# Performance work log

Hardware: AMD Instinct MI355X
Metric: run time of the kernel (lower is better)

## Reference

```python
import jax, jax.numpy as jnp
import numpy as np

BS, H, S, D = 2, 16, 4096, 64
BLOCK = 64
STRIDE_C = 3
NEG = -10000.0


def _global_index(seq_len, block_size, stride_c):
    # static Longformer-style global pattern: first token of each block plus
    # the last `stride_c` tokens of each block
    r = np.arange(seq_len)
    rem = r % block_size
    return np.nonzero((rem == 0) | (rem >= block_size - stride_c))[0]


def setup_inputs() -> dict:
    key = jax.random.key(0)
    k1, k2, k3 = jax.random.split(key, 3)
    q = jax.random.normal(k1, (BS, H, S, D), dtype=jnp.float32)
    k = jax.random.normal(k2, (BS, H, S, D), dtype=jnp.float32)
    v = jax.random.normal(k3, (BS, H, S, D), dtype=jnp.float32)
    mask = jnp.ones((BS, S), dtype=jnp.float32)  # all tokens valid -> pattern is static
    return {"query": q, "key": k, "value": v, "mask": mask}


def reference(query, key, value, mask):
    bs, h, S, d = query.shape
    block = BLOCK
    nb = S // block  # seq_len chosen as multiple of block_size, so pad_len == 0
    g_idx = jnp.asarray(_global_index(S, block, STRIDE_C))  # [G]

    # ---- block-local attention scores ----
    bq = query.reshape(bs, h, nb, block, d)
    bk = key.reshape(bs, h, nb, block, d)
    local = jnp.einsum('bhnxd,bhnyd->bhnxy', bq, bk)  # [bs,h,nb,block,block]
    # additive key-side mask (per key position within each block)
    key_mask = jnp.where(mask == 0.0, NEG, 0.0).reshape(bs, 1, nb, 1, block)
    local = (local + key_mask).reshape(bs, h, S, block)

    # ---- global-token attention scores ----
    gk = key[:, :, g_idx, :]    # [bs,h,G,d]
    gv = value[:, :, g_idx, :]  # [bs,h,G,d]
    gscores = jnp.einsum('bhsd,bhgd->bhsg', query, gk)  # [bs,h,S,G]
    gmask = jnp.where(mask[:, g_idx] == 0.0, NEG, 0.0)[:, None, None, :]
    gscores = gscores + gmask

    # ---- joint softmax over [local block | global tokens] ----
    scores = jnp.concatenate([local, gscores], axis=-1)  # [bs,h,S,block+G]
    probs = jax.nn.softmax(scores.astype(jnp.float32), axis=-1)

    # ---- weighted sums ----
    lp = probs[..., :block].reshape(bs, h, nb, block, block)
    bv = value.reshape(bs, h, nb, block, d)
    lout = jnp.matmul(lp, bv).reshape(bs, h, S, d)
    gout = jnp.einsum('bhsg,bhgd->bhsd', probs[..., block:], gv)
    return lout + gout
```

## Files before the change

kernel.cpp:

```cpp
#include <hip/hip_runtime.h>

#define NEGV -10000.0f

typedef _Float16 f16x8 __attribute__((ext_vector_type(8)));
typedef _Float16 f16x2 __attribute__((ext_vector_type(2)));
typedef float floatx4 __attribute__((ext_vector_type(4)));

__device__ __forceinline__ int src_row(int key, int nblk) {
    if (key < 64) return nblk * 64 + key;
    int g = key - 64;
    int p = g & 3;
    return (g >> 2) * 64 + (p ? (60 + p) : 0);
}

__global__ __launch_bounds__(256, 4)
void sparse_attn_kernel(const float* __restrict__ Q, const float* __restrict__ K,
                        const float* __restrict__ V, const float* __restrict__ M,
                        float* __restrict__ O)
{
    const int x    = blockIdx.x;
    const int bh   = (x & 7) * 4 + ((x >> 3) >> 6);
    const int nblk = (x >> 3) & 63;
    const int b    = bh >> 4;

    const size_t hoff = (size_t)bh * (4096 * 64);
    const float* Qh = Q + hoff;
    const float* Kh = K + hoff;
    const float* Vh = V + hoff;
    float*       Oh = O + hoff;
    const float* Mb = M + (size_t)b * 4096;

    __shared__ _Float16 smem[20480];
    _Float16* Pbase  = smem;
    _Float16* VTbase = smem + 10240;

    const int tid  = threadIdx.x;
    const int lane = tid & 63;
    const int wv   = tid >> 6;
    const int m    = lane & 15;
    const int quad = lane >> 4;
    const int sgl  = lane ^ (lane >> 2);
    const int cg   = lane & 15;
    const int ppb  = ((wv << 2) + (lane >> 4) + ((cg >> 2) << 2)) & 15;

    float mv[5];
    #pragma unroll
    for (int s = 0; s < 5; ++s)
        mv[s] = (Mb[src_row(s * 64 + lane, nblk)] == 0.0f) ? NEGV : 0.0f;

    const int qrow = nblk * 64 + wv * 16 + m;
    f16x8 qf[2];
    #pragma unroll
    for (int c = 0; c < 2; ++c) {
        const float* src = Qh + (size_t)qrow * 64 + c * 32 + quad * 8;
        float4 f0 = *(const float4*)src;
        float4 f1 = *(const float4*)(src + 4);
        qf[c][0] = (_Float16)f0.x; qf[c][1] = (_Float16)f0.y;
        qf[c][2] = (_Float16)f0.z; qf[c][3] = (_Float16)f0.w;
        qf[c][4] = (_Float16)f1.x; qf[c][5] = (_Float16)f1.y;
        qf[c][6] = (_Float16)f1.z; qf[c][7] = (_Float16)f1.w;
    }

    #pragma unroll
    for (int it = 0; it < 10; ++it) {
        int S    = it * 256 + tid;
        int row  = ((S >> 7) * 16) + (S & 15);
        int col0 = ((S >> 6) & 1) * 32 + ((S & 63) >> 4) * 8;
        const float* src = Kh + (size_t)src_row(row, nblk) * 64 + col0;
        float4 f0 = *(const float4*)src;
        float4 f1 = *(const float4*)(src + 4);
        f16x8 o;
        o[0] = (_Float16)f0.x; o[1] = (_Float16)f0.y;
        o[2] = (_Float16)f0.z; o[3] = (_Float16)f0.w;
        o[4] = (_Float16)f1.x; o[5] = (_Float16)f1.y;
        o[6] = (_Float16)f1.z; o[7] = (_Float16)f1.w;
        *(f16x8*)(&smem[S * 8]) = o;
    }

    __syncthreads();

    floatx4 acc[20];
    #pragma unroll
    for (int t = 0; t < 20; ++t) {
        float ma = __shfl(mv[t >> 2], (t & 3) * 16 + m, 64);
        acc[t][0] = ma; acc[t][1] = ma; acc[t][2] = ma; acc[t][3] = ma;
    }
    #pragma unroll
    for (int t = 0; t < 20; ++t) {
        #pragma unroll
        for (int c = 0; c < 2; ++c) {
            f16x8 kf = *(const f16x8*)(&smem[(t * 2 + c) * 512 + lane * 8]);
            acc[t] = __builtin_amdgcn_mfma_f32_16x16x32_f16(qf[c], kf, acc[t], 0, 0, 0);
        }
    }

    float rmax[4] = {-3e38f, -3e38f, -3e38f, -3e38f};
    #pragma unroll
    for (int t = 0; t < 20; ++t)
        #pragma unroll
        for (int r = 0; r < 4; ++r)
            rmax[r] = fmaxf(rmax[r], acc[t][r]);
    #pragma unroll
    for (int off = 8; off >= 1; off >>= 1)
        #pragma unroll
        for (int r = 0; r < 4; ++r)
            rmax[r] = fmaxf(rmax[r], __shfl_xor(rmax[r], off, 64));
    float rsum[4] = {0.f, 0.f, 0.f, 0.f};
    #pragma unroll
    for (int t = 0; t < 20; ++t)
        #pragma unroll
        for (int r = 0; r < 4; ++r) {
            float e = __expf(acc[t][r] - rmax[r]);
            acc[t][r] = e;
            rsum[r] += e;
        }
    #pragma unroll
    for (int off = 8; off >= 1; off >>= 1)
        #pragma unroll
        for (int r = 0; r < 4; ++r)
            rsum[r] += __shfl_xor(rsum[r], off, 64);
    float rinv[4];
    #pragma unroll
    for (int r = 0; r < 4; ++r) rinv[r] = 1.0f / rsum[r];

    __syncthreads();

    #pragma unroll
    for (int tp = 0; tp < 10; ++tp) {
        int slab = wv * 5 + (tp >> 1);
        int gb   = ((tp & 1) * 2 + (m >> 3)) * 16 + quad * 4;
        #pragma unroll
        for (int r = 0; r < 4; ++r) {
            int g  = gb + r;
            int sg = g ^ (g >> 2);
            Pbase[slab * 512 + sg * 8 + (m & 7)] = (_Float16)acc[tp][r];
        }
    }
    #pragma unroll
    for (int s = 0; s < 5; ++s) {
        int rl = 2 * (s * 16 + ppb);
        float4 f0 = *(const float4*)(Vh + (size_t)src_row(rl,     nblk) * 64 + cg * 4);
        float4 f1 = *(const float4*)(Vh + (size_t)src_row(rl + 1, nblk) * 64 + cg * 4);
        int slab = (cg >> 2) * 5 + (rl >> 5);
        int gq   = ((rl & 31) >> 3) * 16;
        int j0   = rl & 7;
        f16x2 pk[4];
        pk[0][0] = (_Float16)f0.x; pk[0][1] = (_Float16)f1.x;
        pk[1][0] = (_Float16)f0.y; pk[1][1] = (_Float16)f1.y;
        pk[2][0] = (_Float16)f0.z; pk[2][1] = (_Float16)f1.z;
        pk[3][0] = (_Float16)f0.w; pk[3][1] = (_Float16)f1.w;
        #pragma unroll
        for (int e = 0; e < 4; ++e) {
            int g  = gq + (cg & 3) * 4 + e;
            int sg = g ^ (g >> 2);
            *(f16x2*)(&VTbase[slab * 512 + sg * 8 + j0]) = pk[e];
        }
    }

    __syncthreads();

    floatx4 oacc[4] = {};
    #pragma unroll
    for (int kc = 0; kc < 5; ++kc) {
        f16x8 pf = *(const f16x8*)(&Pbase[(wv * 5 + kc) * 512 + sgl * 8]);
        #pragma unroll
        for (int t = 0; t < 4; ++t) {
            f16x8 vf = *(const f16x8*)(&VTbase[(t * 5 + kc) * 512 + sgl * 8]);
            oacc[t] = __builtin_amdgcn_mfma_f32_16x16x32_f16(pf, vf, oacc[t], 0, 0, 0);
        }
    }

    __syncthreads();

    #pragma unroll
    for (int tp = 0; tp < 10; ++tp) {
        int slab = wv * 5 + (tp >> 1);
        int gb   = ((tp & 1) * 2 + (m >> 3)) * 16 + quad * 4;
        #pragma unroll
        for (int r = 0; r < 4; ++r) {
            int g  = gb + r;
            int sg = g ^ (g >> 2);
            Pbase[slab * 512 + sg * 8 + (m & 7)] = (_Float16)acc[10 + tp][r];
        }
    }
    #pragma unroll
    for (int s = 0; s < 5; ++s) {
        int rl  = 2 * (s * 16 + ppb);
        int key = 160 + rl;
        float4 f0 = *(const float4*)(Vh + (size_t)src_row(key,     nblk) * 64 + cg * 4);
        float4 f1 = *(const float4*)(Vh + (size_t)src_row(key + 1, nblk) * 64 + cg * 4);
        int slab = (cg >> 2) * 5 + (rl >> 5);
        int gq   = ((rl & 31) >> 3) * 16;
        int j0   = rl & 7;
        f16x2 pk[4];
        pk[0][0] = (_Float16)f0.x; pk[0][1] = (_Float16)f1.x;
        pk[1][0] = (_Float16)f0.y; pk[1][1] = (_Float16)f1.y;
        pk[2][0] = (_Float16)f0.z; pk[2][1] = (_Float16)f1.z;
        pk[3][0] = (_Float16)f0.w; pk[3][1] = (_Float16)f1.w;
        #pragma unroll
        for (int e = 0; e < 4; ++e) {
            int g  = gq + (cg & 3) * 4 + e;
            int sg = g ^ (g >> 2);
            *(f16x2*)(&VTbase[slab * 512 + sg * 8 + j0]) = pk[e];
        }
    }

    __syncthreads();

    #pragma unroll
    for (int kc = 0; kc < 5; ++kc) {
        f16x8 pf = *(const f16x8*)(&Pbase[(wv * 5 + kc) * 512 + sgl * 8]);
        #pragma unroll
        for (int t = 0; t < 4; ++t) {
            f16x8 vf = *(const f16x8*)(&VTbase[(t * 5 + kc) * 512 + sgl * 8]);
            oacc[t] = __builtin_amdgcn_mfma_f32_16x16x32_f16(pf, vf, oacc[t], 0, 0, 0);
        }
    }

    #pragma unroll
    for (int t = 0; t < 4; ++t)
        #pragma unroll
        for (int r = 0; r < 4; ++r)
            Oh[(size_t)(nblk * 64 + wv * 16 + quad * 4 + r) * 64 + t * 16 + m] =
                oacc[t][r] * rinv[r];
}

extern "C" void kernel_launch(void* const* d_in, const int* in_sizes, int n_in,
                              void* d_out, int out_size, void* d_ws, size_t ws_size,
                              hipStream_t stream) {
    const float* q    = (const float*)d_in[0];
    const float* k    = (const float*)d_in[1];
    const float* v    = (const float*)d_in[2];
    const float* mask = (const float*)d_in[3];
    float* out = (float*)d_out;
    (void)in_sizes; (void)n_in; (void)out_size; (void)d_ws; (void)ws_size;
    sparse_attn_kernel<<<2 * 16 * 64, 256, 0, stream>>>(q, k, v, mask, out);
}
```

Measured before the change: 161.6 us.

## Compute transposed scores so probabilities feed PV MFMA directly from registers

Swaps the MFMA operand order so each lane holds a full query row of scores. The softmax row reductions then become two cross-quad shuffles, and the fp16 probabilities can be packed straight into MFMA A-fragments without going through shared memory. V is prefetched into registers earlier and written into a single swizzled transposed LDS layout covering all 320 keys, which removes two LDS round trips and several barriers. The mask add is skipped through a ballot when no key is masked. Launch bounds are relaxed from 4 to 3 to allow more registers per thread, at the risk of lower occupancy.

```diff
diff --git a/kernel.cpp b/kernel.cpp
--- a/kernel.cpp
+++ b/kernel.cpp
@@ -13,7 +13,7 @@
     return (g >> 2) * 64 + (p ? (60 + p) : 0);
 }
 
-__global__ __launch_bounds__(256, 4)
+__global__ __launch_bounds__(256, 3)
 void sparse_attn_kernel(const float* __restrict__ Q, const float* __restrict__ K,
                         const float* __restrict__ V, const float* __restrict__ M,
                         float* __restrict__ O)
@@ -31,22 +31,23 @@
     const float* Mb = M + (size_t)b * 4096;
 
     __shared__ _Float16 smem[20480];
-    _Float16* Pbase  = smem;
-    _Float16* VTbase = smem + 10240;
 
     const int tid  = threadIdx.x;
     const int lane = tid & 63;
     const int wv   = tid >> 6;
     const int m    = lane & 15;
     const int quad = lane >> 4;
-    const int sgl  = lane ^ (lane >> 2);
-    const int cg   = lane & 15;
-    const int ppb  = ((wv << 2) + (lane >> 4) + ((cg >> 2) << 2)) & 15;
-
-    float mv[5];
-    #pragma unroll
-    for (int s = 0; s < 5; ++s)
-        mv[s] = (Mb[src_row(s * 64 + lane, nblk)] == 0.0f) ? NEGV : 0.0f;
+    const int cg   = tid & 15;
+    const int pg   = tid >> 4;
+
+    float mv2[5];
+    unsigned long long bb = 0ull;
+    #pragma unroll
+    for (int s = 0; s < 5; ++s) {
+        float mval = Mb[src_row(s * 64 + lane, nblk)];
+        bb |= __ballot(mval == 0.0f);
+        mv2[s] = (mval == 0.0f) ? NEGV : 0.0f;
+    }
 
     const int qrow = nblk * 64 + wv * 16 + m;
     f16x8 qf[2];
@@ -64,9 +65,11 @@
     #pragma unroll
     for (int it = 0; it < 10; ++it) {
         int S    = it * 256 + tid;
-        int row  = ((S >> 7) * 16) + (S & 15);
+        int t    = S >> 7;
+        int n    = S & 15;
         int col0 = ((S >> 6) & 1) * 32 + ((S & 63) >> 4) * 8;
-        const float* src = Kh + (size_t)src_row(row, nblk) * 64 + col0;
+        int lkey = 32 * (t >> 1) + 8 * (n >> 2) + 4 * (t & 1) + (n & 3);
+        const float* src = Kh + (size_t)src_row(lkey, nblk) * 64 + col0;
         float4 f0 = *(const float4*)src;
         float4 f1 = *(const float4*)(src + 4);
         f16x8 o;
@@ -77,152 +80,124 @@
         *(f16x8*)(&smem[S * 8]) = o;
     }
 
+    float4 v0a[5], v0b[5];
+    #pragma unroll
+    for (int it = 0; it < 5; ++it) {
+        int l0 = 2 * (it * 16 + pg);
+        v0a[it] = *(const float4*)(Vh + (size_t)src_row(l0,     nblk) * 64 + cg * 4);
+        v0b[it] = *(const float4*)(Vh + (size_t)src_row(l0 + 1, nblk) * 64 + cg * 4);
+    }
+
     __syncthreads();
 
-    floatx4 acc[20];
-    #pragma unroll
-    for (int t = 0; t < 20; ++t) {
-        float ma = __shfl(mv[t >> 2], (t & 3) * 16 + m, 64);
-        acc[t][0] = ma; acc[t][1] = ma; acc[t][2] = ma; acc[t][3] = ma;
-    }
+    floatx4 acc[20] = {};
     #pragma unroll
     for (int t = 0; t < 20; ++t) {
         #pragma unroll
         for (int c = 0; c < 2; ++c) {
             f16x8 kf = *(const f16x8*)(&smem[(t * 2 + c) * 512 + lane * 8]);
-            acc[t] = __builtin_amdgcn_mfma_f32_16x16x32_f16(qf[c], kf, acc[t], 0, 0, 0);
-        }
-    }
-
-    float rmax[4] = {-3e38f, -3e38f, -3e38f, -3e38f};
+            acc[t] = __builtin_amdgcn_mfma_f32_16x16x32_f16(kf, qf[c], acc[t], 0, 0, 0);
+        }
+    }
+
+    __syncthreads();
+
+    auto vt_store = [&](int l0, const float4& f0, const float4& f1) {
+        int kc2   = l0 >> 5;
+        int q2    = (l0 & 31) >> 3;
+        int j0    = l0 & 7;
+        int td    = cg >> 2;
+        int sw    = td << 4;
+        int lbase = (kc2 * 4 + td) * 512 + q2 * 128 + (cg & 3) * 32 + j0;
+        f16x2 pk0; pk0[0] = (_Float16)f0.x; pk0[1] = (_Float16)f1.x;
+        *(f16x2*)(&smem[(lbase +  0) ^ sw]) = pk0;
+        f16x2 pk1; pk1[0] = (_Float16)f0.y; pk1[1] = (_Float16)f1.y;
+        *(f16x2*)(&smem[(lbase +  8) ^ sw]) = pk1;
+        f16x2 pk2; pk2[0] = (_Float16)f0.z; pk2[1] = (_Float16)f1.z;
+        *(f16x2*)(&smem[(lbase + 16) ^ sw]) = pk2;
+        f16x2 pk3; pk3[0] = (_Float16)f0.w; pk3[1] = (_Float16)f1.w;
+        *(f16x2*)(&smem[(lbase + 24) ^ sw]) = pk3;
+    };
+
+    #pragma unroll
+    for (int it = 0; it < 5; ++it)
+        vt_store(2 * (it * 16 + pg), v0a[it], v0b[it]);
+
+    float4 v1a[5], v1b[5];
+    #pragma unroll
+    for (int it = 0; it < 5; ++it) {
+        int l0 = 2 * ((5 + it) * 16 + pg);
+        v1a[it] = *(const float4*)(Vh + (size_t)src_row(l0,     nblk) * 64 + cg * 4);
+        v1b[it] = *(const float4*)(Vh + (size_t)src_row(l0 + 1, nblk) * 64 + cg * 4);
+    }
+
+    if (bb != 0ull) {
+        #pragma unroll
+        for (int t = 0; t < 20; ++t) {
+            int lb = 32 * ((t >> 1) & 1) + 4 * (t & 1) + 8 * quad;
+            #pragma unroll
+            for (int r = 0; r < 4; ++r)
+                acc[t][r] += __shfl(mv2[t >> 2], lb + r, 64);
+        }
+    }
+
+    float rmax = -3e38f;
     #pragma unroll
     for (int t = 0; t < 20; ++t)
         #pragma unroll
         for (int r = 0; r < 4; ++r)
-            rmax[r] = fmaxf(rmax[r], acc[t][r]);
-    #pragma unroll
-    for (int off = 8; off >= 1; off >>= 1)
-        #pragma unroll
-        for (int r = 0; r < 4; ++r)
-            rmax[r] = fmaxf(rmax[r], __shfl_xor(rmax[r], off, 64));
-    float rsum[4] = {0.f, 0.f, 0.f, 0.f};
+            rmax = fmaxf(rmax, acc[t][r]);
+    rmax = fmaxf(rmax, __shfl_xor(rmax, 16, 64));
+    rmax = fmaxf(rmax, __shfl_xor(rmax, 32, 64));
+    float rsum = 0.f;
     #pragma unroll
     for (int t = 0; t < 20; ++t)
         #pragma unroll
         for (int r = 0; r < 4; ++r) {
-            float e = __expf(acc[t][r] - rmax[r]);
+            float e = __expf(acc[t][r] - rmax);
             acc[t][r] = e;
-            rsum[r] += e;
-        }
-    #pragma unroll
-    for (int off = 8; off >= 1; off >>= 1)
-        #pragma unroll
-        for (int r = 0; r < 4; ++r)
-            rsum[r] += __shfl_xor(rsum[r], off, 64);
-    float rinv[4];
-    #pragma unroll
-    for (int r = 0; r < 4; ++r) rinv[r] = 1.0f / rsum[r];
+            rsum += e;
+        }
+    rsum += __shfl_xor(rsum, 16, 64);
+    rsum += __shfl_xor(rsum, 32, 64);
+    float rinv = 1.0f / rsum;
+
+    #pragma unroll
+    for (int it = 0; it < 5; ++it)
+        vt_store(2 * ((5 + it) * 16 + pg), v1a[it], v1b[it]);
+
+    f16x8 pf[10];
+    #pragma unroll
+    for (int k2 = 0; k2 < 10; ++k2) {
+        #pragma unroll
+        for (int r = 0; r < 4; ++r) {
+            pf[k2][r]     = (_Float16)acc[2 * k2][r];
+            pf[k2][4 + r] = (_Float16)acc[2 * k2 + 1][r];
+        }
+    }
 
     __syncthreads();
 
-    #pragma unroll
-    for (int tp = 0; tp < 10; ++tp) {
-        int slab = wv * 5 + (tp >> 1);
-        int gb   = ((tp & 1) * 2 + (m >> 3)) * 16 + quad * 4;
-        #pragma unroll
-        for (int r = 0; r < 4; ++r) {
-            int g  = gb + r;
-            int sg = g ^ (g >> 2);
-            Pbase[slab * 512 + sg * 8 + (m & 7)] = (_Float16)acc[tp][r];
-        }
-    }
-    #pragma unroll
-    for (int s = 0; s < 5; ++s) {
-        int rl = 2 * (s * 16 + ppb);
-        float4 f0 = *(const float4*)(Vh + (size_t)src_row(rl,     nblk) * 64 + cg * 4);
-        float4 f1 = *(const float4*)(Vh + (size_t)src_row(rl + 1, nblk) * 64 + cg * 4);
-        int slab = (cg >> 2) * 5 + (rl >> 5);
-        int gq   = ((rl & 31) >> 3) * 16;
-        int j0   = rl & 7;
-        f16x2 pk[4];
-        pk[0][0] = (_Float16)f0.x; pk[0][1] = (_Float16)f1.x;
-        pk[1][0] = (_Float16)f0.y; pk[1][1] = (_Float16)f1.y;
-        pk[2][0] = (_Float16)f0.z; pk[2][1] = (_Float16)f1.z;
-        pk[3][0] = (_Float16)f0.w; pk[3][1] = (_Float16)f1.w;
-        #pragma unroll
-        for (int e = 0; e < 4; ++e) {
-            int g  = gq + (cg & 3) * 4 + e;
-            int sg = g ^ (g >> 2);
-            *(f16x2*)(&VTbase[slab * 512 + sg * 8 + j0]) = pk[e];
-        }
-    }
-
-    __syncthreads();
-
     floatx4 oacc[4] = {};
     #pragma unroll
-    for (int kc = 0; kc < 5; ++kc) {
-        f16x8 pf = *(const f16x8*)(&Pbase[(wv * 5 + kc) * 512 + sgl * 8]);
+    for (int k2 = 0; k2 < 10; ++k2) {
         #pragma unroll
         for (int t = 0; t < 4; ++t) {
-            f16x8 vf = *(const f16x8*)(&VTbase[(t * 5 + kc) * 512 + sgl * 8]);
-            oacc[t] = __builtin_amdgcn_mfma_f32_16x16x32_f16(pf, vf, oacc[t], 0, 0, 0);
-        }
-    }
-
-    __syncthreads();
-
-    #pragma unroll
-    for (int tp = 0; tp < 10; ++tp) {
-        int slab = wv * 5 + (tp >> 1);
-        int gb   = ((tp & 1) * 2 + (m >> 3)) * 16 + quad * 4;
-        #pragma unroll
-        for (int r = 0; r < 4; ++r) {
-            int g  = gb + r;
-            int sg = g ^ (g >> 2);
-            Pbase[slab * 512 + sg * 8 + (m & 7)] = (_Float16)acc[10 + tp][r];
-        }
-    }
-    #pragma unroll
-    for (int s = 0; s < 5; ++s) {
-        int rl  = 2 * (s * 16 + ppb);
-        int key = 160 + rl;
-        float4 f0 = *(const float4*)(Vh + (size_t)src_row(key,     nblk) * 64 + cg * 4);
-        float4 f1 = *(const float4*)(Vh + (size_t)src_row(key + 1, nblk) * 64 + cg * 4);
-        int slab = (cg >> 2) * 5 + (rl >> 5);
-        int gq   = ((rl & 31) >> 3) * 16;
-        int j0   = rl & 7;
-        f16x2 pk[4];
-        pk[0][0] = (_Float16)f0.x; pk[0][1] = (_Float16)f1.x;
-        pk[1][0] = (_Float16)f0.y; pk[1][1] = (_Float16)f1.y;
-        pk[2][0] = (_Float16)f0.z; pk[2][1] = (_Float16)f1.z;
-        pk[3][0] = (_Float16)f0.w; pk[3][1] = (_Float16)f1.w;
-        #pragma unroll
-        for (int e = 0; e < 4; ++e) {
-            int g  = gq + (cg & 3) * 4 + e;
-            int sg = g ^ (g >> 2);
-            *(f16x2*)(&VTbase[slab * 512 + sg * 8 + j0]) = pk[e];
-        }
-    }
-
-    __syncthreads();
-
-    #pragma unroll
-    for (int kc = 0; kc < 5; ++kc) {
-        f16x8 pf = *(const f16x8*)(&Pbase[(wv * 5 + kc) * 512 + sgl * 8]);
-        #pragma unroll
-        for (int t = 0; t < 4; ++t) {
-            f16x8 vf = *(const f16x8*)(&VTbase[(t * 5 + kc) * 512 + sgl * 8]);
-            oacc[t] = __builtin_amdgcn_mfma_f32_16x16x32_f16(pf, vf, oacc[t], 0, 0, 0);
-        }
-    }
-
+            f16x8 vf = *(const f16x8*)(&smem[(k2 * 4 + t) * 512 + ((lane * 8) ^ (t << 4))]);
+            oacc[t] = __builtin_amdgcn_mfma_f32_16x16x32_f16(pf[k2], vf, oacc[t], 0, 0, 0);
+        }
+    }
+
+    float rinvr[4];
+    #pragma unroll
+    for (int r = 0; r < 4; ++r)
+        rinvr[r] = __shfl(rinv, quad * 4 + r, 64);
     #pragma unroll
     for (int t = 0; t < 4; ++t)
         #pragma unroll
         for (int r = 0; r < 4; ++r)
             Oh[(size_t)(nblk * 64 + wv * 16 + quad * 4 + r) * 64 + t * 16 + m] =
-                oacc[t][r] * rinv[r];
+                oacc[t][r] * rinvr[r];
 }
 
 extern "C" void kernel_launch(void* const* d_in, const int* in_sizes, int n_in,
```

Result: faster. 156.8 us (-3.0%).
